# Performance work log

Hardware: AMD Instinct MI355X
Metric: run time of the kernel (lower is better)

## Reference

```python
import jax, jax.numpy as jnp
import numpy as np

DT = 0.01
OMEGA_MAX = 100.0


def setup_inputs() -> dict:
    key = jax.random.key(0)
    ks = jax.random.split(key, 7)
    B, T, D, M = 4, 4096, 1024, 64
    N = 2 * M
    u = jax.random.normal(ks[0], (B, T, D), dtype=jnp.float32)
    W_omega = jax.random.normal(ks[1], (M, D), dtype=jnp.float32) * 0.02
    b_omega = jnp.ones((M,), dtype=jnp.float32)
    W_zeta = jax.random.normal(ks[2], (M, D), dtype=jnp.float32) * 0.02
    b_zeta = jnp.zeros((M,), dtype=jnp.float32)
    W_B = jax.random.normal(ks[3], (N, D), dtype=jnp.float32) * (0.1 / np.sqrt(D))
    b_B = jnp.zeros((N,), dtype=jnp.float32)
    C = jax.random.normal(ks[4], (D, N), dtype=jnp.float32) * 0.01
    D_mat = jax.random.normal(ks[5], (D, D), dtype=jnp.float32) * 0.01
    return dict(u=u, W_omega=W_omega, b_omega=b_omega, W_zeta=W_zeta,
                b_zeta=b_zeta, W_B=W_B, b_B=b_B, C=C, D_mat=D_mat)


def reference(u, W_omega, b_omega, W_zeta, b_zeta, W_B, b_B, C, D_mat):
    B, T, D = u.shape
    M = W_omega.shape[0]
    # Hoist all per-step linear projections into batched GEMMs (same math).
    omega = jax.nn.softplus(jnp.einsum('btd,md->btm', u, W_omega) + b_omega)
    omega = jnp.clip(omega, 1e-4, OMEGA_MAX)                      # (B,T,M)
    zeta = jax.nn.sigmoid(jnp.einsum('btd,md->btm', u, W_zeta) + b_zeta)
    A = omega * omega                                             # (B,T,M)
    S = 1.0 / (1.0 + (DT * DT) * A)                               # (B,T,M)
    d = 1.0 - zeta                                                # (B,T,M)
    F = jnp.einsum('btd,nd->btn', u, W_B) + b_B                   # (B,T,2M)

    def step(x, inp):
        A_t, S_t, d_t, F_t = inp                                  # (B,M)x3, (B,2M)
        z = x[:, :M]
        y = x[:, M:]
        z_new = d_t * (S_t * z - DT * A_t * S_t * y)
        y_new = d_t * (DT * S_t * z + S_t * y)
        x_new = jnp.concatenate([z_new, y_new], axis=-1) + F_t
        return x_new, x_new

    x0 = jnp.zeros((B, 2 * M), dtype=u.dtype)
    tm = lambda a: jnp.swapaxes(a, 0, 1)  # to time-major for scan
    _, xs = jax.lax.scan(step, x0, (tm(A), tm(S), tm(d), tm(F)))
    xs = jnp.swapaxes(xs, 0, 1)                                   # (B,T,2M)
    # Output projection: y_t = x_t C^T + u_t D^T
    y = jnp.einsum('btn,dn->btd', xs, C) + jnp.einsum('bte,de->btd', u, D_mat)
    return y
```

## Files before the change

kernel.cpp:

```cpp
#include <hip/hip_runtime.h>
#include <hip/hip_bf16.h>
#include <math.h>

#define DTC 0.01f

typedef __attribute__((ext_vector_type(8))) short short8;
typedef __attribute__((ext_vector_type(4))) float f32x4;
typedef unsigned short bf16raw;

__device__ __forceinline__ bf16raw f2bf(float f){
  union { unsigned u; float f; } v; v.f = f;
  unsigned r = v.u + 0x7FFF + ((v.u >> 16) & 1u);
  return (bf16raw)(r >> 16);
}

__device__ __forceinline__ short8 ld8f(const float* __restrict__ p){
  float4 a = *(const float4*)p;
  float4 b = *(const float4*)(p + 4);
  short8 r;
  r[0] = (short)f2bf(a.x); r[1] = (short)f2bf(a.y);
  r[2] = (short)f2bf(a.z); r[3] = (short)f2bf(a.w);
  r[4] = (short)f2bf(b.x); r[5] = (short)f2bf(b.y);
  r[6] = (short)f2bf(b.z); r[7] = (short)f2bf(b.w);
  return r;
}

template<int ITERS>
__device__ __forceinline__ void stage_async(const bf16raw* __restrict__ src, long ld,
                                            long row0, int k0, bf16raw* lds,
                                            int wave, int lane){
  int kchunk = (lane & 3) ^ ((lane >> 3) & 3);
#pragma unroll
  for (int i = 0; i < ITERS; ++i){
    int r0 = (wave*ITERS + i) * 16;
    long row = row0 + r0 + (lane >> 2);
    const bf16raw* gp = src + row*ld + k0 + kchunk*8;
    bf16raw* lp = lds + r0*32;
    __builtin_amdgcn_global_load_lds((const __attribute__((address_space(1))) void*)gp,
                                     (__attribute__((address_space(3))) void*)lp,
                                     16, 0, 0);
  }
}

template<int MI, int NI>
__device__ __forceinline__ void mma_tile(const bf16raw* Alds, const bf16raw* Blds,
                                         f32x4 acc[MI][NI], int wm, int wn, int quad, int t16){
  short8 af[MI], bfr[NI];
  int sw = (quad ^ ((t16 >> 1) & 3)) * 8;
#pragma unroll
  for (int mi = 0; mi < MI; ++mi)
    af[mi] = *(const short8*)(Alds + (wm*(MI*16) + mi*16 + t16)*32 + sw);
#pragma unroll
  for (int ni = 0; ni < NI; ++ni)
    bfr[ni] = *(const short8*)(Blds + (wn*(NI*16) + ni*16 + t16)*32 + sw);
#pragma unroll
  for (int mi = 0; mi < MI; ++mi)
#pragma unroll
    for (int ni = 0; ni < NI; ++ni)
      acc[mi][ni] = __builtin_amdgcn_mfma_f32_16x16x32_bf16(af[mi], bfr[ni], acc[mi][ni], 0, 0, 0);
}

extern "C" __global__ void k_prep(const float* __restrict__ u,
    const float* __restrict__ Wom, const float* __restrict__ Wze,
    const float* __restrict__ WB, const float* __restrict__ Cm,
    const float* __restrict__ Dm, bf16raw* __restrict__ u_bf,
    bf16raw* __restrict__ Wcat, bf16raw* __restrict__ C_bf,
    bf16raw* __restrict__ Dm_bf){
  long g = (long)blockIdx.x * 256 + threadIdx.x;
  const float* src; bf16raw* dst; long o;
  if      (g < 2097152){ src = u;   dst = u_bf;          o = g; }
  else if (g < 2105344){ src = Wom; dst = Wcat;          o = g - 2097152; }
  else if (g < 2113536){ src = Wze; dst = Wcat + 65536;  o = g - 2105344; }
  else if (g < 2129920){ src = WB;  dst = Wcat + 131072; o = g - 2113536; }
  else if (g < 2146304){ src = Cm;  dst = C_bf;          o = g - 2129920; }
  else                 { src = Dm;  dst = Dm_bf;         o = g - 2146304; }
  *(short8*)(dst + o*8) = ld8f(src + o*8);
}

extern "C" __global__ __launch_bounds__(256) void k_gemm_p(
    const bf16raw* __restrict__ u_bf, const bf16raw* __restrict__ Wcat,
    float* __restrict__ P){
  __shared__ __align__(16) bf16raw Alds[3*64*32];
  __shared__ __align__(16) bf16raw Blds[3*128*32];
  int tid = threadIdx.x, wave = tid >> 6, lane = tid & 63;
  int quad = lane >> 4, t16 = lane & 15;
  int wm = wave >> 1, wn = wave & 1;
  int id  = blockIdx.y * gridDim.x + blockIdx.x;
  int sid = (id & 7) * 64 + (id >> 3);
  long row0 = (long)(sid >> 1) * 64;
  int  col0 = (sid & 1) * 128;
  f32x4 acc[2][4] = {};

  auto stage = [&](int kt, int buf){
    stage_async<1>(u_bf, 1024, row0, kt*32, Alds + buf*(64*32), wave, lane);
    stage_async<2>(Wcat, 1024, col0, kt*32, Blds + buf*(128*32), wave, lane);
  };

  stage(0, 0);
  stage(1, 1);
  int rd = 0;
  for (int s = 0; s < 30; ++s){
    asm volatile("s_waitcnt vmcnt(3)" ::: "memory");
    __builtin_amdgcn_s_barrier();
    __builtin_amdgcn_sched_barrier(0);
    int st = rd >= 1 ? rd - 1 : 2;
    stage(s + 2, st);
    __builtin_amdgcn_s_setprio(1);
    mma_tile<2,4>(Alds + rd*(64*32), Blds + rd*(128*32), acc, wm, wn, quad, t16);
    __builtin_amdgcn_s_setprio(0);
    rd = rd < 2 ? rd + 1 : 0;
  }
  asm volatile("s_waitcnt vmcnt(3)" ::: "memory");
  __builtin_amdgcn_s_barrier();
  __builtin_amdgcn_sched_barrier(0);
  mma_tile<2,4>(Alds + 0*(64*32), Blds + 0*(128*32), acc, wm, wn, quad, t16);
  asm volatile("s_waitcnt vmcnt(0)" ::: "memory");
  __builtin_amdgcn_s_barrier();
  __builtin_amdgcn_sched_barrier(0);
  mma_tile<2,4>(Alds + 1*(64*32), Blds + 1*(128*32), acc, wm, wn, quad, t16);
#pragma unroll
  for (int mi = 0; mi < 2; ++mi)
#pragma unroll
    for (int ni = 0; ni < 4; ++ni)
#pragma unroll
      for (int r = 0; r < 4; ++r){
        long grow = row0 + wm*32 + mi*16 + quad*4 + r;
        int  gcol = col0 + wn*64 + ni*16 + t16;
        P[grow*256 + gcol] = acc[mi][ni][r];
      }
}

extern "C" __global__ __launch_bounds__(256, 2) void k_gemm_out(
    const bf16raw* __restrict__ Xs, const bf16raw* __restrict__ u_bf,
    const bf16raw* __restrict__ C_bf, const bf16raw* __restrict__ Dm_bf,
    float* __restrict__ out){
  __shared__ __align__(16) bf16raw Alds[3*128*32];
  __shared__ __align__(16) bf16raw Blds[3*256*32];
  int tid = threadIdx.x, wave = tid >> 6, lane = tid & 63;
  int quad = lane >> 4, t16 = lane & 15;
  int wm = wave >> 1, wn = wave & 1;
  int id  = blockIdx.y * gridDim.x + blockIdx.x;
  int sid = (id & 7) * 64 + (id >> 3);
  long row0 = (long)(sid >> 2) * 128;
  int  col0 = (sid & 3) * 256;
  f32x4 acc[4][8] = {};

  auto stage = [&](int s, int buf){
    if (s < 4){
      stage_async<2>(Xs,   128, row0, s*32, Alds + buf*(128*32), wave, lane);
      stage_async<4>(C_bf, 128, col0, s*32, Blds + buf*(256*32), wave, lane);
    } else {
      stage_async<2>(u_bf,  1024, row0, (s-4)*32, Alds + buf*(128*32), wave, lane);
      stage_async<4>(Dm_bf, 1024, col0, (s-4)*32, Blds + buf*(256*32), wave, lane);
    }
  };

  stage(0, 0);
  stage(1, 1);
  int rd = 0;
  for (int s = 0; s < 34; ++s){
    asm volatile("s_waitcnt vmcnt(6)" ::: "memory");
    __builtin_amdgcn_s_barrier();
    __builtin_amdgcn_sched_barrier(0);
    int st = rd >= 1 ? rd - 1 : 2;
    stage(s + 2, st);
    __builtin_amdgcn_s_setprio(1);
    mma_tile<4,8>(Alds + rd*(128*32), Blds + rd*(256*32), acc, wm, wn, quad, t16);
    __builtin_amdgcn_s_setprio(0);
    rd = rd < 2 ? rd + 1 : 0;
  }
  asm volatile("s_waitcnt vmcnt(6)" ::: "memory");
  __builtin_amdgcn_s_barrier();
  __builtin_amdgcn_sched_barrier(0);
  mma_tile<4,8>(Alds + 1*(128*32), Blds + 1*(256*32), acc, wm, wn, quad, t16);
  asm volatile("s_waitcnt vmcnt(0)" ::: "memory");
  __builtin_amdgcn_s_barrier();
  __builtin_amdgcn_sched_barrier(0);
  mma_tile<4,8>(Alds + 2*(128*32), Blds + 2*(256*32), acc, wm, wn, quad, t16);
#pragma unroll
  for (int mi = 0; mi < 4; ++mi)
#pragma unroll
    for (int ni = 0; ni < 8; ++ni)
#pragma unroll
      for (int r = 0; r < 4; ++r){
        long grow = row0 + wm*64 + mi*16 + quad*4 + r;
        int  gcol = col0 + wn*128 + ni*16 + t16;
        out[grow*1024 + gcol] = acc[mi][ni][r];
      }
}

extern "C" __global__ __launch_bounds__(256) void k_scanA(
    const float* __restrict__ P, const float* __restrict__ b_om,
    const float* __restrict__ b_ze, const float* __restrict__ b_B,
    float4* __restrict__ Coef, float4* __restrict__ CM, float2* __restrict__ CV){
  int tid = threadIdx.x, c = blockIdx.x;
  int b = tid >> 6, m = tid & 63;
  float bo = b_om[m], bz = b_ze[m], bb0 = b_B[m], bb1 = b_B[64 + m];
  const float* row = P + ((size_t)b*4096 + c*16) * 256;
  float4* cf = Coef + ((size_t)b*4096 + c*16) * 64 + m;
  float m00=1.f, m01=0.f, m10=0.f, m11=0.f, vz=0.f, vy=0.f;
#pragma unroll 4
  for (int t = 0; t < 16; ++t){
    const float* r = row + t*256;
    float wo = r[m]       + bo;
    float wz = r[64 + m]  + bz;
    float fz = r[128 + m] + bb0;
    float fy = r[192 + m] + bb1;
    float sp = (wo > 20.f) ? wo : log1pf(expf(wo));
    float omega = fminf(fmaxf(sp, 1e-4f), 100.f);
    float A = omega * omega;
    float S = 1.f / (1.f + DTC*DTC*A);
    float zeta = 1.f / (1.f + expf(-wz));
    float p = (1.f - zeta) * S;
    float q = p * DTC * A;
    cf[t*64] = make_float4(p, q, fz, fy);
    float nvz = p*vz - q*vy + fz;
    float nvy = DTC*p*vz + p*vy + fy;
    vz = nvz; vy = nvy;
    float n00 = p*m00 - q*m10;
    float n01 = p*m01 - q*m11;
    float n10 = DTC*p*m00 + p*m10;
    float n11 = DTC*p*m01 + p*m11;
    m00=n00; m01=n01; m10=n10; m11=n11;
  }
  CM[c*256 + tid] = make_float4(m00, m01, m10, m11);
  CV[c*256 + tid] = make_float2(vz, vy);
}

extern "C" __global__ __launch_bounds__(256) void k_scanC(
    const float4* __restrict__ Coef, const float4* __restrict__ CM,
    const float2* __restrict__ CV, bf16raw* __restrict__ Xs){
  int tid = threadIdx.x, c = blockIdx.x;
  int b = tid >> 6, m = tid & 63;
  float xz = 0.f, xy = 0.f;
#pragma unroll 4
  for (int j = 0; j < c; ++j){
    float4 Mv = CM[j*256 + tid];
    float2 Vv = CV[j*256 + tid];
    float nz = Mv.x*xz + Mv.y*xy + Vv.x;
    float ny = Mv.z*xz + Mv.w*xy + Vv.y;
    xz = nz; xy = ny;
  }
  const float4* cf = Coef + ((size_t)b*4096 + c*16) * 64 + m;
  bf16raw* xp = Xs + ((size_t)b*4096 + c*16) * 128 + m;
#pragma unroll 4
  for (int t = 0; t < 16; ++t){
    float4 f = cf[t*64];
    float nz = f.x*xz - f.y*xy + f.z;
    float ny = DTC*f.x*xz + f.x*xy + f.w;
    xz = nz; xy = ny;
    xp[t*128]      = f2bf(xz);
    xp[t*128 + 64] = f2bf(xy);
  }
}

extern "C" void kernel_launch(void* const* d_in, const int* in_sizes, int n_in,
                              void* d_out, int out_size, void* d_ws, size_t ws_size,
                              hipStream_t stream){
  const float* u   = (const float*)d_in[0];
  const float* Wom = (const float*)d_in[1];
  const float* bom = (const float*)d_in[2];
  const float* Wze = (const float*)d_in[3];
  const float* bze = (const float*)d_in[4];
  const float* WB  = (const float*)d_in[5];
  const float* bB  = (const float*)d_in[6];
  const float* Cm  = (const float*)d_in[7];
  const float* Dm  = (const float*)d_in[8];
  float* out = (float*)d_out;

  char* ws = (char*)d_ws;
  size_t off = 0;
  bf16raw* u_bf  = (bf16raw*)(ws + off); off += (size_t)16777216*2;
  bf16raw* Wcat  = (bf16raw*)(ws + off); off += (size_t)262144*2;
  bf16raw* C_bf  = (bf16raw*)(ws + off); off += (size_t)131072*2;
  bf16raw* Dm_bf = (bf16raw*)(ws + off); off += (size_t)1048576*2;
  float*   P     = (float*)  (ws + off);
  bf16raw* Xs    = (bf16raw*)P;
  off += (size_t)16384*256*4;
  float4*  Coef  = (float4*) (ws + off); off += (size_t)16384*64*16;
  float4*  CMw   = (float4*) (ws + off); off += (size_t)256*256*16;
  float2*  CVw   = (float2*) (ws + off); off += (size_t)256*256*8;

  k_prep    <<<8896, 256, 0, stream>>>(u, Wom, Wze, WB, Cm, Dm, u_bf, Wcat, C_bf, Dm_bf);
  k_gemm_p  <<<dim3(2, 256), 256, 0, stream>>>(u_bf, Wcat, P);
  k_scanA   <<<256, 256, 0, stream>>>(P, bom, bze, bB, Coef, CMw, CVw);
  k_scanC   <<<256, 256, 0, stream>>>(Coef, CMw, CVw, Xs);
  k_gemm_out<<<dim3(4, 128), 256, 0, stream>>>(Xs, u_bf, C_bf, Dm_bf, out);
}
```

Measured before the change: 231.5 us.

## Shrink GEMM tiles for more blocks and recompute scan coefficients instead of storing

Both GEMM kernels now use smaller output tiles: 64x64 for the projection GEMM and 128x128 for the output GEMM. Launch grids double and occupancy hints rise, so more blocks fill the CUs. The scan no longer writes the per-step coefficient array in the first pass. The second pass recomputes softplus and sigmoid from P, trading a 16 MB store and reload for extra transcendental math. The smaller tiles lower per-block data reuse and so raise L2/LDS traffic.

```diff
diff --git a/kernel.cpp b/kernel.cpp
--- a/kernel.cpp
+++ b/kernel.cpp
@@ -77,114 +77,114 @@
   *(short8*)(dst + o*8) = ld8f(src + o*8);
 }
 
-extern "C" __global__ __launch_bounds__(256) void k_gemm_p(
+extern "C" __global__ __launch_bounds__(256, 4) void k_gemm_p(
     const bf16raw* __restrict__ u_bf, const bf16raw* __restrict__ Wcat,
     float* __restrict__ P){
   __shared__ __align__(16) bf16raw Alds[3*64*32];
+  __shared__ __align__(16) bf16raw Blds[3*64*32];
+  int tid = threadIdx.x, wave = tid >> 6, lane = tid & 63;
+  int quad = lane >> 4, t16 = lane & 15;
+  int wm = wave >> 1, wn = wave & 1;
+  int id  = blockIdx.y * gridDim.x + blockIdx.x;
+  int sid = (id & 7) * 128 + (id >> 3);
+  long row0 = (long)(sid >> 2) * 64;
+  int  col0 = (sid & 3) * 64;
+  f32x4 acc[2][2] = {};
+
+  auto stage = [&](int kt, int buf){
+    stage_async<1>(u_bf, 1024, row0, kt*32, Alds + buf*(64*32), wave, lane);
+    stage_async<1>(Wcat, 1024, col0, kt*32, Blds + buf*(64*32), wave, lane);
+  };
+
+  stage(0, 0);
+  stage(1, 1);
+  int rd = 0;
+  for (int s = 0; s < 30; ++s){
+    asm volatile("s_waitcnt vmcnt(2)" ::: "memory");
+    __builtin_amdgcn_s_barrier();
+    __builtin_amdgcn_sched_barrier(0);
+    int st = rd >= 1 ? rd - 1 : 2;
+    stage(s + 2, st);
+    __builtin_amdgcn_s_setprio(1);
+    mma_tile<2,2>(Alds + rd*(64*32), Blds + rd*(64*32), acc, wm, wn, quad, t16);
+    __builtin_amdgcn_s_setprio(0);
+    rd = rd < 2 ? rd + 1 : 0;
+  }
+  asm volatile("s_waitcnt vmcnt(2)" ::: "memory");
+  __builtin_amdgcn_s_barrier();
+  __builtin_amdgcn_sched_barrier(0);
+  mma_tile<2,2>(Alds + 0*(64*32), Blds + 0*(64*32), acc, wm, wn, quad, t16);
+  asm volatile("s_waitcnt vmcnt(0)" ::: "memory");
+  __builtin_amdgcn_s_barrier();
+  __builtin_amdgcn_sched_barrier(0);
+  mma_tile<2,2>(Alds + 1*(64*32), Blds + 1*(64*32), acc, wm, wn, quad, t16);
+#pragma unroll
+  for (int mi = 0; mi < 2; ++mi)
+#pragma unroll
+    for (int ni = 0; ni < 2; ++ni)
+#pragma unroll
+      for (int r = 0; r < 4; ++r){
+        long grow = row0 + wm*32 + mi*16 + quad*4 + r;
+        int  gcol = col0 + wn*32 + ni*16 + t16;
+        P[grow*256 + gcol] = acc[mi][ni][r];
+      }
+}
+
+extern "C" __global__ __launch_bounds__(256, 3) void k_gemm_out(
+    const bf16raw* __restrict__ Xs, const bf16raw* __restrict__ u_bf,
+    const bf16raw* __restrict__ C_bf, const bf16raw* __restrict__ Dm_bf,
+    float* __restrict__ out){
+  __shared__ __align__(16) bf16raw Alds[3*128*32];
   __shared__ __align__(16) bf16raw Blds[3*128*32];
   int tid = threadIdx.x, wave = tid >> 6, lane = tid & 63;
   int quad = lane >> 4, t16 = lane & 15;
   int wm = wave >> 1, wn = wave & 1;
   int id  = blockIdx.y * gridDim.x + blockIdx.x;
-  int sid = (id & 7) * 64 + (id >> 3);
-  long row0 = (long)(sid >> 1) * 64;
-  int  col0 = (sid & 1) * 128;
-  f32x4 acc[2][4] = {};
-
-  auto stage = [&](int kt, int buf){
-    stage_async<1>(u_bf, 1024, row0, kt*32, Alds + buf*(64*32), wave, lane);
-    stage_async<2>(Wcat, 1024, col0, kt*32, Blds + buf*(128*32), wave, lane);
+  int sid = (id & 7) * 128 + (id >> 3);
+  long row0 = (long)(sid >> 3) * 128;
+  int  col0 = (sid & 7) * 128;
+  f32x4 acc[4][4] = {};
+
+  auto stage = [&](int s, int buf){
+    if (s < 4){
+      stage_async<2>(Xs,   128, row0, s*32, Alds + buf*(128*32), wave, lane);
+      stage_async<2>(C_bf, 128, col0, s*32, Blds + buf*(128*32), wave, lane);
+    } else {
+      stage_async<2>(u_bf,  1024, row0, (s-4)*32, Alds + buf*(128*32), wave, lane);
+      stage_async<2>(Dm_bf, 1024, col0, (s-4)*32, Blds + buf*(128*32), wave, lane);
+    }
   };
 
   stage(0, 0);
   stage(1, 1);
   int rd = 0;
-  for (int s = 0; s < 30; ++s){
-    asm volatile("s_waitcnt vmcnt(3)" ::: "memory");
+  for (int s = 0; s < 34; ++s){
+    asm volatile("s_waitcnt vmcnt(4)" ::: "memory");
     __builtin_amdgcn_s_barrier();
     __builtin_amdgcn_sched_barrier(0);
     int st = rd >= 1 ? rd - 1 : 2;
     stage(s + 2, st);
     __builtin_amdgcn_s_setprio(1);
-    mma_tile<2,4>(Alds + rd*(64*32), Blds + rd*(128*32), acc, wm, wn, quad, t16);
+    mma_tile<4,4>(Alds + rd*(128*32), Blds + rd*(128*32), acc, wm, wn, quad, t16);
     __builtin_amdgcn_s_setprio(0);
     rd = rd < 2 ? rd + 1 : 0;
   }
-  asm volatile("s_waitcnt vmcnt(3)" ::: "memory");
-  __builtin_amdgcn_s_barrier();
-  __builtin_amdgcn_sched_barrier(0);
-  mma_tile<2,4>(Alds + 0*(64*32), Blds + 0*(128*32), acc, wm, wn, quad, t16);
+  asm volatile("s_waitcnt vmcnt(4)" ::: "memory");
+  __builtin_amdgcn_s_barrier();
+  __builtin_amdgcn_sched_barrier(0);
+  mma_tile<4,4>(Alds + 1*(128*32), Blds + 1*(128*32), acc, wm, wn, quad, t16);
   asm volatile("s_waitcnt vmcnt(0)" ::: "memory");
   __builtin_amdgcn_s_barrier();
   __builtin_amdgcn_sched_barrier(0);
-  mma_tile<2,4>(Alds + 1*(64*32), Blds + 1*(128*32), acc, wm, wn, quad, t16);
-#pragma unroll
-  for (int mi = 0; mi < 2; ++mi)
+  mma_tile<4,4>(Alds + 2*(128*32), Blds + 2*(128*32), acc, wm, wn, quad, t16);
+#pragma unroll
+  for (int mi = 0; mi < 4; ++mi)
 #pragma unroll
     for (int ni = 0; ni < 4; ++ni)
-#pragma unroll
-      for (int r = 0; r < 4; ++r){
-        long grow = row0 + wm*32 + mi*16 + quad*4 + r;
-        int  gcol = col0 + wn*64 + ni*16 + t16;
-        P[grow*256 + gcol] = acc[mi][ni][r];
-      }
-}
-
-extern "C" __global__ __launch_bounds__(256, 2) void k_gemm_out(
-    const bf16raw* __restrict__ Xs, const bf16raw* __restrict__ u_bf,
-    const bf16raw* __restrict__ C_bf, const bf16raw* __restrict__ Dm_bf,
-    float* __restrict__ out){
-  __shared__ __align__(16) bf16raw Alds[3*128*32];
-  __shared__ __align__(16) bf16raw Blds[3*256*32];
-  int tid = threadIdx.x, wave = tid >> 6, lane = tid & 63;
-  int quad = lane >> 4, t16 = lane & 15;
-  int wm = wave >> 1, wn = wave & 1;
-  int id  = blockIdx.y * gridDim.x + blockIdx.x;
-  int sid = (id & 7) * 64 + (id >> 3);
-  long row0 = (long)(sid >> 2) * 128;
-  int  col0 = (sid & 3) * 256;
-  f32x4 acc[4][8] = {};
-
-  auto stage = [&](int s, int buf){
-    if (s < 4){
-      stage_async<2>(Xs,   128, row0, s*32, Alds + buf*(128*32), wave, lane);
-      stage_async<4>(C_bf, 128, col0, s*32, Blds + buf*(256*32), wave, lane);
-    } else {
-      stage_async<2>(u_bf,  1024, row0, (s-4)*32, Alds + buf*(128*32), wave, lane);
-      stage_async<4>(Dm_bf, 1024, col0, (s-4)*32, Blds + buf*(256*32), wave, lane);
-    }
-  };
-
-  stage(0, 0);
-  stage(1, 1);
-  int rd = 0;
-  for (int s = 0; s < 34; ++s){
-    asm volatile("s_waitcnt vmcnt(6)" ::: "memory");
-    __builtin_amdgcn_s_barrier();
-    __builtin_amdgcn_sched_barrier(0);
-    int st = rd >= 1 ? rd - 1 : 2;
-    stage(s + 2, st);
-    __builtin_amdgcn_s_setprio(1);
-    mma_tile<4,8>(Alds + rd*(128*32), Blds + rd*(256*32), acc, wm, wn, quad, t16);
-    __builtin_amdgcn_s_setprio(0);
-    rd = rd < 2 ? rd + 1 : 0;
-  }
-  asm volatile("s_waitcnt vmcnt(6)" ::: "memory");
-  __builtin_amdgcn_s_barrier();
-  __builtin_amdgcn_sched_barrier(0);
-  mma_tile<4,8>(Alds + 1*(128*32), Blds + 1*(256*32), acc, wm, wn, quad, t16);
-  asm volatile("s_waitcnt vmcnt(0)" ::: "memory");
-  __builtin_amdgcn_s_barrier();
-  __builtin_amdgcn_sched_barrier(0);
-  mma_tile<4,8>(Alds + 2*(128*32), Blds + 2*(256*32), acc, wm, wn, quad, t16);
-#pragma unroll
-  for (int mi = 0; mi < 4; ++mi)
-#pragma unroll
-    for (int ni = 0; ni < 8; ++ni)
 #pragma unroll
       for (int r = 0; r < 4; ++r){
         long grow = row0 + wm*64 + mi*16 + quad*4 + r;
-        int  gcol = col0 + wn*128 + ni*16 + t16;
+        int  gcol = col0 + wn*64 + ni*16 + t16;
         out[grow*1024 + gcol] = acc[mi][ni][r];
       }
 }
@@ -192,12 +192,11 @@
 extern "C" __global__ __launch_bounds__(256) void k_scanA(
     const float* __restrict__ P, const float* __restrict__ b_om,
     const float* __restrict__ b_ze, const float* __restrict__ b_B,
-    float4* __restrict__ Coef, float4* __restrict__ CM, float2* __restrict__ CV){
+    float4* __restrict__ CM, float2* __restrict__ CV){
   int tid = threadIdx.x, c = blockIdx.x;
   int b = tid >> 6, m = tid & 63;
   float bo = b_om[m], bz = b_ze[m], bb0 = b_B[m], bb1 = b_B[64 + m];
   const float* row = P + ((size_t)b*4096 + c*16) * 256;
-  float4* cf = Coef + ((size_t)b*4096 + c*16) * 64 + m;
   float m00=1.f, m01=0.f, m10=0.f, m11=0.f, vz=0.f, vy=0.f;
 #pragma unroll 4
   for (int t = 0; t < 16; ++t){
@@ -213,7 +212,6 @@
     float zeta = 1.f / (1.f + expf(-wz));
     float p = (1.f - zeta) * S;
     float q = p * DTC * A;
-    cf[t*64] = make_float4(p, q, fz, fy);
     float nvz = p*vz - q*vy + fz;
     float nvy = DTC*p*vz + p*vy + fy;
     vz = nvz; vy = nvy;
@@ -228,8 +226,10 @@
 }
 
 extern "C" __global__ __launch_bounds__(256) void k_scanC(
-    const float4* __restrict__ Coef, const float4* __restrict__ CM,
-    const float2* __restrict__ CV, bf16raw* __restrict__ Xs){
+    const float* __restrict__ P, const float* __restrict__ b_om,
+    const float* __restrict__ b_ze, const float* __restrict__ b_B,
+    const float4* __restrict__ CM, const float2* __restrict__ CV,
+    bf16raw* __restrict__ Xs){
   int tid = threadIdx.x, c = blockIdx.x;
   int b = tid >> 6, m = tid & 63;
   float xz = 0.f, xy = 0.f;
@@ -241,13 +241,25 @@
     float ny = Mv.z*xz + Mv.w*xy + Vv.y;
     xz = nz; xy = ny;
   }
-  const float4* cf = Coef + ((size_t)b*4096 + c*16) * 64 + m;
+  float bo = b_om[m], bz = b_ze[m], bb0 = b_B[m], bb1 = b_B[64 + m];
+  const float* row = P + ((size_t)b*4096 + c*16) * 256;
   bf16raw* xp = Xs + ((size_t)b*4096 + c*16) * 128 + m;
 #pragma unroll 4
   for (int t = 0; t < 16; ++t){
-    float4 f = cf[t*64];
-    float nz = f.x*xz - f.y*xy + f.z;
-    float ny = DTC*f.x*xz + f.x*xy + f.w;
+    const float* r = row + t*256;
+    float wo = r[m]       + bo;
+    float wz = r[64 + m]  + bz;
+    float fz = r[128 + m] + bb0;
+    float fy = r[192 + m] + bb1;
+    float sp = (wo > 20.f) ? wo : log1pf(expf(wo));
+    float omega = fminf(fmaxf(sp, 1e-4f), 100.f);
+    float A = omega * omega;
+    float S = 1.f / (1.f + DTC*DTC*A);
+    float zeta = 1.f / (1.f + expf(-wz));
+    float p = (1.f - zeta) * S;
+    float q = p * DTC * A;
+    float nz = p*xz - q*xy + fz;
+    float ny = DTC*p*xz + p*xy + fy;
     xz = nz; xy = ny;
     xp[t*128]      = f2bf(xz);
     xp[t*128 + 64] = f2bf(xy);
@@ -274,16 +286,14 @@
   bf16raw* Wcat  = (bf16raw*)(ws + off); off += (size_t)262144*2;
   bf16raw* C_bf  = (bf16raw*)(ws + off); off += (size_t)131072*2;
   bf16raw* Dm_bf = (bf16raw*)(ws + off); off += (size_t)1048576*2;
-  float*   P     = (float*)  (ws + off);
-  bf16raw* Xs    = (bf16raw*)P;
-  off += (size_t)16384*256*4;
-  float4*  Coef  = (float4*) (ws + off); off += (size_t)16384*64*16;
+  float*   P     = (float*)  (ws + off); off += (size_t)16384*256*4;
+  bf16raw* Xs    = (bf16raw*)(ws + off); off += (size_t)16384*128*2;
   float4*  CMw   = (float4*) (ws + off); off += (size_t)256*256*16;
   float2*  CVw   = (float2*) (ws + off); off += (size_t)256*256*8;
 
   k_prep    <<<8896, 256, 0, stream>>>(u, Wom, Wze, WB, Cm, Dm, u_bf, Wcat, C_bf, Dm_bf);
-  k_gemm_p  <<<dim3(2, 256), 256, 0, stream>>>(u_bf, Wcat, P);
-  k_scanA   <<<256, 256, 0, stream>>>(P, bom, bze, bB, Coef, CMw, CVw);
-  k_scanC   <<<256, 256, 0, stream>>>(Coef, CMw, CVw, Xs);
-  k_gemm_out<<<dim3(4, 128), 256, 0, stream>>>(Xs, u_bf, C_bf, Dm_bf, out);
-}
+  k_gemm_p  <<<dim3(4, 256), 256, 0, stream>>>(u_bf, Wcat, P);
+  k_scanA   <<<256, 256, 0, stream>>>(P, bom, bze, bB, CMw, CVw);
+  k_scanC   <<<256, 256, 0, stream>>>(P, bom, bze, bB, CMw, CVw, Xs);
+  k_gemm_out<<<dim3(8, 128), 256, 0, stream>>>(Xs, u_bf, C_bf, Dm_bf, out);
+}
```

New measurement: 240.4 us. 3.8% more time.
